# Optimization experiments

Hardware: AMD Instinct MI355X
Metric: run time of the kernel (lower is better)

Reference implementation:

```python
import jax, jax.numpy as jnp
import numpy as np

B = 16384      # batch (rollout size)
OBS = 64       # obs_dim
ACT = 8        # action_dim
H = 128        # hidden_dim
NN = 4         # num_neighbors
N = NN + 1     # num_nodes in local graph
HEADS = 2
SLOPE = 0.2    # leaky_relu negative slope


def setup_inputs() -> dict:
    key = jax.random.key(0)
    ks = jax.random.split(key, 20)

    def glorot(k, shape):
        fan_in, fan_out = shape[0], shape[-1]
        lim = np.sqrt(6.0 / (fan_in + fan_out)).astype(np.float32)
        return jax.random.uniform(k, shape, jnp.float32, -lim, lim)

    obs = jax.random.normal(ks[0], (B, OBS), jnp.float32)
    neighbor_obs = jax.random.normal(ks[1], (B, NN, OBS), jnp.float32)
    adj = jax.random.randint(ks[2], (B, N), 0, 2, jnp.int32)
    adj = adj.at[:, 0].set(1)  # self node always connected (avoids all -inf rows)

    params = dict(
        enc_w1=glorot(ks[3], (OBS, H)), enc_b1=jnp.zeros((H,), jnp.float32),
        enc_w2=glorot(ks[4], (H, H)),  enc_b2=jnp.zeros((H,), jnp.float32),
        gat_w=glorot(ks[5], (HEADS, H, H)),       # per-head W (no bias)
        gat_a=glorot(ks[6], (HEADS, 2 * H)),      # per-head attention vector a
        val_w1=glorot(ks[7], (H * HEADS, H)), val_b1=jnp.zeros((H,), jnp.float32),
        val_w2=glorot(ks[8], (H, 1)),          val_b2=jnp.zeros((1,), jnp.float32),
        pol_w1=glorot(ks[9], (H * HEADS, H)), pol_b1=jnp.zeros((H,), jnp.float32),
        pol_w2=glorot(ks[10], (H, ACT)),       pol_b2=jnp.zeros((ACT,), jnp.float32),
    )
    return {"obs": obs, "neighbor_obs": neighbor_obs, "adj": adj, **params}


def reference(obs, neighbor_obs, adj,
              enc_w1, enc_b1, enc_w2, enc_b2,
              gat_w, gat_a,
              val_w1, val_b1, val_w2, val_b2,
              pol_w1, pol_b1, pol_w2, pol_b2):
    # shared local encoder applied to self obs and each neighbor obs
    all_obs = jnp.concatenate([obs[:, None, :], neighbor_obs], axis=1)   # [B,N,OBS]
    emb = jax.nn.relu(all_obs @ enc_w1 + enc_b1) @ enc_w2 + enc_b2       # [B,N,H]

    # GAT layer (all heads vectorized). Concat attention a^T[Wh_i||Wh_j]
    # decomposes into a1.Wh_i + a2.Wh_j.
    Wh = jnp.einsum('bnd,hdo->bhno', emb, gat_w)                          # [B,heads,N,H]
    a1, a2 = gat_a[:, :H], gat_a[:, H:]
    ei = jnp.einsum('bhno,ho->bhn', Wh, a1)                               # [B,heads,N]
    ej = jnp.einsum('bhno,ho->bhn', Wh, a2)
    e = jax.nn.leaky_relu(ei[..., :, None] + ej[..., None, :], SLOPE)     # [B,heads,N,N]
    # torch masked_fill broadcasts adj [B,N] as a column mask over j
    e = jnp.where((adj == 0)[:, None, None, :], -jnp.inf, e)
    attn = jax.nn.softmax(e, axis=-1)                                     # [B,heads,N,N]
    h_prime = jnp.einsum('bhij,bhjo->bhio', attn, Wh)                     # [B,heads,N,H]

    # node 0 (the agent itself), heads concatenated (head-major order, as torch cat)
    final = h_prime[:, :, 0, :].reshape(h_prime.shape[0], HEADS * H)      # [B,heads*H]

    value = jax.nn.relu(final @ val_w1 + val_b1) @ val_w2 + val_b2        # [B,1]
    logits = jax.nn.relu(final @ pol_w1 + pol_b1) @ pol_w2 + pol_b2      # [B,ACT]
    return value, logits
```

## Files before the change

### kernel.cpp

```cpp
#include <hip/hip_runtime.h>
#include <hip/hip_bf16.h>

#define B_TOT 16384

typedef __attribute__((ext_vector_type(8))) short short8;
typedef __attribute__((ext_vector_type(4))) short short4v;
typedef __attribute__((ext_vector_type(4))) float f32x4;

__device__ __forceinline__ float bf2f(short s){
  unsigned u = ((unsigned)(unsigned short)s) << 16;
  return __uint_as_float(u);
}
__device__ __forceinline__ unsigned f2bfu(float f){
  __hip_bfloat16 h = __float2bfloat16(f);
  return (unsigned)*reinterpret_cast<unsigned short*>(&h);
}
__device__ __forceinline__ short f2bf(float f){
  __hip_bfloat16 h = __float2bfloat16(f);
  return *reinterpret_cast<short*>(&h);
}

#define MFMA16(a,b,c) __builtin_amdgcn_mfma_f32_16x16x32_bf16(a,b,c,0,0,0)

#define W_W1T   0
#define W_W2T   8192
#define W_GWT   24576
#define W_HW1T  57344
#define W_PW2T  122880
#define W_VW2   123904
#define W_NELEM 124032
#define CVEC_BYTE 248064
#define PREP_TOT  124544

__global__ void prep_weights(const float* __restrict__ enc_w1, const float* __restrict__ enc_w2,
                             const float* __restrict__ gat_w, const float* __restrict__ gat_a,
                             const float* __restrict__ val_w1, const float* __restrict__ pol_w1,
                             const float* __restrict__ pol_w2, const float* __restrict__ val_w2,
                             unsigned short* __restrict__ wt, float* __restrict__ cvec){
  int t = blockIdx.x*256 + threadIdx.x;
  if (t >= PREP_TOT) return;
  if (t < W_NELEM){
    float v; int idx;
    if (t < 8192){
      int c = t >> 6, k = t & 63;
      int G = c >> 5, r = c & 31, b = r & 1, f = r >> 1;
      idx = ((G*2 + b)*16 + f)*64 + k;
      v = enc_w1[k*128 + c];
    } else if (t < 24576){
      int u = t - 8192, c = u >> 7, k = u & 127;
      int G = c >> 5, r = c & 31, b = r & 1, f = r >> 1;
      idx = 8192 + ((G*2 + b)*16 + f)*128 + k;
      v = enc_w2[k*128 + c];
    } else if (t < 57344){
      int u = t - 24576, h = u >> 14, r2 = u & 16383, o = r2 >> 7, d = r2 & 127;
      int G = o >> 5, r = o & 31, b = r & 1, f = r >> 1;
      idx = 24576 + h*16384 + ((G*2 + b)*16 + f)*128 + d;
      v = gat_w[h*16384 + d*128 + o];
    } else if (t < 122880){
      int u = t - 57344, oc = u >> 8, k = u & 255;
      int G = oc >> 5, r = oc & 31, b = r & 1, f = r >> 1;
      idx = 57344 + ((G*2 + b)*16 + f)*256 + k;
      v = (oc < 128) ? val_w1[k*128 + oc] : pol_w1[k*128 + (oc - 128)];
    } else if (t < 123904){
      int u = t - 122880, a = u >> 7, k = u & 127;
      idx = t;
      v = pol_w2[k*8 + a];
    } else {
      idx = t;
      v = val_w2[t - 123904];
    }
    wt[idx] = (unsigned short)f2bfu(v);
  } else {
    int q = t - W_NELEM;
    int vsel = q >> 7, d = q & 127;
    int h = vsel >> 1, s2 = vsel & 1;
    const float* gw = gat_w + h*16384 + d*128;
    const float* aa = gat_a + h*256 + s2*128;
    float s = 0.f;
    #pragma unroll 4
    for (int o = 0; o < 128; ++o) s += gw[o]*aa[o];
    cvec[vsel*128 + d] = s;
  }
}

#define MIX_L   20480
#define FINAL_L 0
#define H2_L    8192
#define K_LDS   30720

__global__ __launch_bounds__(256, 4) void colight_fused(
    const float* __restrict__ obs, const float* __restrict__ nobs, const int* __restrict__ adjp,
    const float* __restrict__ enc_b1, const float* __restrict__ enc_b2,
    const float* __restrict__ val_b1, const float* __restrict__ val_b2,
    const float* __restrict__ pol_b1, const float* __restrict__ pol_b2,
    const unsigned short* __restrict__ wt_all, const float* __restrict__ cvec,
    float* __restrict__ dout)
{
  __shared__ __align__(16) char lds[K_LDS];
  const int tid  = threadIdx.x;
  const int lane = tid & 63;
  const int wv   = tid >> 6;
  const int lm   = lane & 15;
  const int grp  = lane >> 4;
  const int kb   = grp * 8;
  const int gblk = blockIdx.x * 16;

  const unsigned short* w1t  = wt_all + W_W1T;
  const unsigned short* w2t  = wt_all + W_W2T;
  const unsigned short* gwt  = wt_all + W_GWT;
  const unsigned short* hw1t = wt_all + W_HW1T;
  const unsigned short* pw2t = wt_all + W_PW2T;
  const unsigned short* vw2  = wt_all + W_VW2;

  #pragma unroll
  for (int i = 0; i < 5; ++i){
    int chunk = i*256 + tid;
    int row = chunk >> 4;
    int c4  = (chunk & 15) * 4;
    int a = row/5, n = row%5;
    const float* src = n ? (nobs + ((size_t)(gblk+a)*4 + (n-1))*64 + c4)
                         : (obs  + (size_t)(gblk+a)*64 + c4);
    float4 v = *reinterpret_cast<const float4*>(src);
    short4v p = { f2bf(v.x), f2bf(v.y), f2bf(v.z), f2bf(v.w) };
    *reinterpret_cast<short4v*>(lds + ((row*128 + c4*2) ^ ((row & 7) << 4))) = p;
  }
  __syncthreads();

  {
    f32x4 aE[5], aO[5];
    #pragma unroll
    for (int mt=0; mt<5; ++mt){ aE[mt]=(f32x4){0,0,0,0}; aO[mt]=(f32x4){0,0,0,0}; }
    #pragma unroll
    for (int ks=0; ks<2; ++ks){
      short8 bE = *reinterpret_cast<const short8*>(w1t + ((wv*2+0)*16 + lm)*64 + ks*32 + kb);
      short8 bO = *reinterpret_cast<const short8*>(w1t + ((wv*2+1)*16 + lm)*64 + ks*32 + kb);
      #pragma unroll
      for (int mt=0; mt<5; ++mt){
        int row = mt*16 + lm;
        short8 a = *reinterpret_cast<short8*>(lds + ((row*128 + (ks*32+kb)*2) ^ ((row&7)<<4)));
        aE[mt] = MFMA16(a, bE, aE[mt]);
        aO[mt] = MFMA16(a, bO, aO[mt]);
      }
    }
    const int ce = 32*wv + 2*lm;
    const float be = enc_b1[ce], bo = enc_b1[ce+1];
    #pragma unroll
    for (int mt=0; mt<5; ++mt)
      #pragma unroll
      for (int j=0; j<4; ++j){
        int row = mt*16 + grp*4 + j;
        unsigned pk = f2bfu(fmaxf(aE[mt][j] + be, 0.f))
                    | (f2bfu(fmaxf(aO[mt][j] + bo, 0.f)) << 16);
        *reinterpret_cast<unsigned*>(lds + 10240 + ((row*256 + ce*2) ^ ((row&7)<<4))) = pk;
      }
  }
  __syncthreads();

  {
    f32x4 aE[5], aO[5];
    #pragma unroll
    for (int mt=0; mt<5; ++mt){ aE[mt]=(f32x4){0,0,0,0}; aO[mt]=(f32x4){0,0,0,0}; }
    #pragma unroll
    for (int ks=0; ks<4; ++ks){
      short8 bE = *reinterpret_cast<const short8*>(w2t + ((wv*2+0)*16 + lm)*128 + ks*32 + kb);
      short8 bO = *reinterpret_cast<const short8*>(w2t + ((wv*2+1)*16 + lm)*128 + ks*32 + kb);
      #pragma unroll
      for (int mt=0; mt<5; ++mt){
        int row = mt*16 + lm;
        short8 a = *reinterpret_cast<short8*>(lds + 10240 + ((row*256 + (ks*32+kb)*2) ^ ((row&7)<<4)));
        aE[mt] = MFMA16(a, bE, aE[mt]);
        aO[mt] = MFMA16(a, bO, aO[mt]);
      }
    }
    __syncthreads();
    const int ce = 32*wv + 2*lm;
    const float be = enc_b2[ce], bo = enc_b2[ce+1];
    #pragma unroll
    for (int mt=0; mt<5; ++mt)
      #pragma unroll
      for (int j=0; j<4; ++j){
        int row = mt*16 + grp*4 + j;
        unsigned pk = f2bfu(aE[mt][j] + be) | (f2bfu(aO[mt][j] + bo) << 16);
        *reinterpret_cast<unsigned*>(lds + ((row*256 + ce*2) ^ ((row&7)<<4))) = pk;
      }
  }
  __syncthreads();

  {
    const int ag = wv*4 + grp;
    const int ga = gblk + ag;
    float ef[5][8];
    #pragma unroll
    for (int n=0; n<5; ++n){
      int row = ag*5 + n;
      short8 er = *reinterpret_cast<short8*>(lds + ((row*256 + lm*16) ^ ((row&7)<<4)));
      #pragma unroll
      for (int e=0; e<8; ++e) ef[n][e] = bf2f(er[e]);
    }
    int msk[5];
    #pragma unroll
    for (int n=0; n<5; ++n) msk[n] = adjp[(size_t)ga*5 + n];

    #pragma unroll
    for (int h=0; h<2; ++h){
      float c1v[8], c2v[8];
      #pragma unroll
      for (int e=0; e<8; ++e){
        c1v[e] = cvec[(2*h  )*128 + lm*8 + e];
        c2v[e] = cvec[(2*h+1)*128 + lm*8 + e];
      }
      float ei = 0.f;
      #pragma unroll
      for (int e=0; e<8; ++e) ei += ef[0][e]*c1v[e];
      ei += __shfl_xor(ei,1); ei += __shfl_xor(ei,2); ei += __shfl_xor(ei,4); ei += __shfl_xor(ei,8);

      float at[5]; float mx = -1e30f;
      #pragma unroll
      for (int n=0; n<5; ++n){
        float t = 0.f;
        #pragma unroll
        for (int e=0; e<8; ++e) t += ef[n][e]*c2v[e];
        t += __shfl_xor(t,1); t += __shfl_xor(t,2); t += __shfl_xor(t,4); t += __shfl_xor(t,8);
        float s = ei + t;
        s = (s > 0.f) ? s : 0.2f*s;
        at[n] = s;
        if (msk[n] && s > mx) mx = s;
      }
      float den = 0.f;
      #pragma unroll
      for (int n=0; n<5; ++n){
        float e2 = msk[n] ? __expf(at[n]-mx) : 0.f;
        at[n] = e2; den += e2;
      }
      float inv = 1.f/den;
      short8 o;
      #pragma unroll
      for (int e=0; e<8; ++e){
        float s = 0.f;
        #pragma unroll
        for (int n=0; n<5; ++n) s += at[n]*ef[n][e];
        o[e] = f2bf(s*inv);
      }
      *reinterpret_cast<short8*>(lds + MIX_L + ((ag*512 + (h*128 + lm*8)*2) ^ ((ag&7)<<4))) = o;
    }
  }
  __syncthreads();

  {
    const int hh = wv >> 1, half = wv & 1;
    f32x4 fE[2], fO[2];
    #pragma unroll
    for (int g2=0; g2<2; ++g2){ fE[g2]=(f32x4){0,0,0,0}; fO[g2]=(f32x4){0,0,0,0}; }
    #pragma unroll
    for (int ks=0; ks<4; ++ks){
      short8 a = *reinterpret_cast<short8*>(lds + MIX_L + ((lm*512 + (hh*128 + ks*32 + kb)*2) ^ ((lm&7)<<4)));
      #pragma unroll
      for (int g2=0; g2<2; ++g2){
        int G = half*2 + g2;
        short8 bE = *reinterpret_cast<const short8*>(gwt + hh*16384 + ((G*2+0)*16 + lm)*128 + ks*32 + kb);
        short8 bO = *reinterpret_cast<const short8*>(gwt + hh*16384 + ((G*2+1)*16 + lm)*128 + ks*32 + kb);
        fE[g2] = MFMA16(a, bE, fE[g2]);
        fO[g2] = MFMA16(a, bO, fO[g2]);
      }
    }
    #pragma unroll
    for (int g2=0; g2<2; ++g2){
      int cb = hh*128 + half*64 + 32*g2 + 2*lm;
      #pragma unroll
      for (int j=0; j<4; ++j){
        int row = grp*4 + j;
        unsigned pk = f2bfu(fE[g2][j]) | (f2bfu(fO[g2][j]) << 16);
        *reinterpret_cast<unsigned*>(lds + FINAL_L + ((row*512 + cb*2) ^ ((row&7)<<4))) = pk;
      }
    }
  }
  __syncthreads();

  {
    f32x4 hE[2], hO[2];
    #pragma unroll
    for (int g2=0; g2<2; ++g2){ hE[g2]=(f32x4){0,0,0,0}; hO[g2]=(f32x4){0,0,0,0}; }
    #pragma unroll
    for (int ks=0; ks<8; ++ks){
      short8 a = *reinterpret_cast<short8*>(lds + FINAL_L + ((lm*512 + (ks*32+kb)*2) ^ ((lm&7)<<4)));
      #pragma unroll
      for (int g2=0; g2<2; ++g2){
        int G = 2*wv + g2;
        short8 bE = *reinterpret_cast<const short8*>(hw1t + ((G*2+0)*16 + lm)*256 + ks*32 + kb);
        short8 bO = *reinterpret_cast<const short8*>(hw1t + ((G*2+1)*16 + lm)*256 + ks*32 + kb);
        hE[g2] = MFMA16(a, bE, hE[g2]);
        hO[g2] = MFMA16(a, bO, hO[g2]);
      }
    }
    #pragma unroll
    for (int g2=0; g2<2; ++g2){
      int oc = 64*wv + 32*g2 + 2*lm;
      float be = (oc   < 128) ? val_b1[oc]   : pol_b1[oc-128];
      float bo = (oc+1 < 128) ? val_b1[oc+1] : pol_b1[oc-127];
      #pragma unroll
      for (int j=0; j<4; ++j){
        int row = grp*4 + j;
        unsigned pk = f2bfu(fmaxf(hE[g2][j] + be, 0.f))
                    | (f2bfu(fmaxf(hO[g2][j] + bo, 0.f)) << 16);
        *reinterpret_cast<unsigned*>(lds + H2_L + ((row*512 + oc*2) ^ ((row&7)<<4))) = pk;
      }
    }
  }
  __syncthreads();

  if (tid < 128){
    int a = tid >> 3, act = tid & 7;
    float s = pol_b2[act];
    #pragma unroll
    for (int i=0; i<16; ++i){
      short8 v = *reinterpret_cast<short8*>(lds + H2_L + ((a*512 + (128 + i*8)*2) ^ ((a&7)<<4)));
      short8 w = *reinterpret_cast<const short8*>(pw2t + act*128 + i*8);
      #pragma unroll
      for (int e=0; e<8; ++e) s += bf2f(v[e]) * bf2f(w[e]);
    }
    dout[B_TOT + (size_t)(gblk + a)*8 + act] = s;
  } else if (tid < 160){
    int q = tid - 128, a = q >> 1, hf = q & 1;
    float s = 0.f;
    #pragma unroll
    for (int i=0; i<8; ++i){
      short8 v = *reinterpret_cast<short8*>(lds + H2_L + ((a*512 + (hf*64 + i*8)*2) ^ ((a&7)<<4)));
      short8 w = *reinterpret_cast<const short8*>(vw2 + hf*64 + i*8);
      #pragma unroll
      for (int e=0; e<8; ++e) s += bf2f(v[e]) * bf2f(w[e]);
    }
    s += __shfl_xor(s, 1);
    if (!hf) dout[gblk + a] = s + val_b2[0];
  }
}

extern "C" void kernel_launch(void* const* d_in, const int* in_sizes, int n_in,
                              void* d_out, int out_size, void* d_ws, size_t ws_size,
                              hipStream_t stream) {
  (void)in_sizes; (void)n_in; (void)out_size; (void)ws_size;
  const float* obs    = (const float*)d_in[0];
  const float* nobs   = (const float*)d_in[1];
  const int*   adj    = (const int*)  d_in[2];
  const float* enc_w1 = (const float*)d_in[3];
  const float* enc_b1 = (const float*)d_in[4];
  const float* enc_w2 = (const float*)d_in[5];
  const float* enc_b2 = (const float*)d_in[6];
  const float* gat_w  = (const float*)d_in[7];
  const float* gat_a  = (const float*)d_in[8];
  const float* val_w1 = (const float*)d_in[9];
  const float* val_b1 = (const float*)d_in[10];
  const float* val_w2 = (const float*)d_in[11];
  const float* val_b2 = (const float*)d_in[12];
  const float* pol_w1 = (const float*)d_in[13];
  const float* pol_b1 = (const float*)d_in[14];
  const float* pol_w2 = (const float*)d_in[15];
  const float* pol_b2 = (const float*)d_in[16];

  unsigned short* wt   = (unsigned short*)d_ws;
  float*          cvec = (float*)((char*)d_ws + CVEC_BYTE);

  prep_weights<<<(PREP_TOT + 255)/256, 256, 0, stream>>>(
      enc_w1, enc_w2, gat_w, gat_a, val_w1, pol_w1, pol_w2, val_w2, wt, cvec);

  colight_fused<<<B_TOT/16, 256, 0, stream>>>(
      obs, nobs, adj, enc_b1, enc_b2,
      val_b1, val_b2, pol_b1, pol_b2,
      wt, cvec, (float*)d_out);
}
```

Measured before the change: 136.5 us.

## Halve agents per block to 8, shrink LDS, split heads across lane groups

Each block now processes 8 agents instead of 16, doubling the grid. LDS drops from 30 KB to 15 KB and launch bounds rise to 8 waves per SIMD to raise occupancy. The attention stage assigns one head per 16-lane group instead of looping over both heads. In exchange, the encoder and head GEMMs use padded MFMA tiles: 40 rows are covered by 48 and 8 rows by 16, so some MFMA work is wasted, and weight fragments are reloaded by twice as many blocks.

```diff
diff --git a/kernel.cpp b/kernel.cpp
--- a/kernel.cpp
+++ b/kernel.cpp
@@ -63,11 +63,9 @@
       v = (oc < 128) ? val_w1[k*128 + oc] : pol_w1[k*128 + (oc - 128)];
     } else if (t < 123904){
       int u = t - 122880, a = u >> 7, k = u & 127;
-      idx = t;
-      v = pol_w2[k*8 + a];
+      idx = t; v = pol_w2[k*8 + a];
     } else {
-      idx = t;
-      v = val_w2[t - 123904];
+      idx = t; v = val_w2[t - 123904];
     }
     wt[idx] = (unsigned short)f2bfu(v);
   } else {
@@ -83,12 +81,15 @@
   }
 }
 
-#define MIX_L   20480
-#define FINAL_L 0
-#define H2_L    8192
-#define K_LDS   30720
-
-__global__ __launch_bounds__(256, 4) void colight_fused(
+#define X_L     0
+#define H1_L    5120
+#define EMB_L   0
+#define MIX_L   10240
+#define FIN_L   0
+#define H2_L    4096
+#define K_LDS   15360
+
+__global__ __launch_bounds__(256, 8) void colight_fused(
     const float* __restrict__ obs, const float* __restrict__ nobs, const int* __restrict__ adjp,
     const float* __restrict__ enc_b1, const float* __restrict__ enc_b2,
     const float* __restrict__ val_b1, const float* __restrict__ val_b2,
@@ -103,7 +104,7 @@
   const int lm   = lane & 15;
   const int grp  = lane >> 4;
   const int kb   = grp * 8;
-  const int gblk = blockIdx.x * 16;
+  const int gblk = blockIdx.x * 8;
 
   const unsigned short* w1t  = wt_all + W_W1T;
   const unsigned short* w2t  = wt_all + W_W2T;
@@ -113,31 +114,34 @@
   const unsigned short* vw2  = wt_all + W_VW2;
 
   #pragma unroll
-  for (int i = 0; i < 5; ++i){
+  for (int i = 0; i < 3; ++i){
     int chunk = i*256 + tid;
-    int row = chunk >> 4;
-    int c4  = (chunk & 15) * 4;
-    int a = row/5, n = row%5;
-    const float* src = n ? (nobs + ((size_t)(gblk+a)*4 + (n-1))*64 + c4)
-                         : (obs  + (size_t)(gblk+a)*64 + c4);
-    float4 v = *reinterpret_cast<const float4*>(src);
-    short4v p = { f2bf(v.x), f2bf(v.y), f2bf(v.z), f2bf(v.w) };
-    *reinterpret_cast<short4v*>(lds + ((row*128 + c4*2) ^ ((row & 7) << 4))) = p;
-  }
-  __syncthreads();
-
-  {
-    f32x4 aE[5], aO[5];
-    #pragma unroll
-    for (int mt=0; mt<5; ++mt){ aE[mt]=(f32x4){0,0,0,0}; aO[mt]=(f32x4){0,0,0,0}; }
+    if (chunk < 640){
+      int row = chunk >> 4;
+      int c4  = (chunk & 15) * 4;
+      int a = row/5, n = row%5;
+      const float* src = n ? (nobs + ((size_t)(gblk+a)*4 + (n-1))*64 + c4)
+                           : (obs  + (size_t)(gblk+a)*64 + c4);
+      float4 v = *reinterpret_cast<const float4*>(src);
+      short4v p = { f2bf(v.x), f2bf(v.y), f2bf(v.z), f2bf(v.w) };
+      *reinterpret_cast<short4v*>(lds + X_L + ((row*128 + c4*2) ^ ((row & 7) << 4))) = p;
+    }
+  }
+  __syncthreads();
+
+  {
+    f32x4 aE[3], aO[3];
+    #pragma unroll
+    for (int mt=0; mt<3; ++mt){ aE[mt]=(f32x4){0,0,0,0}; aO[mt]=(f32x4){0,0,0,0}; }
     #pragma unroll
     for (int ks=0; ks<2; ++ks){
       short8 bE = *reinterpret_cast<const short8*>(w1t + ((wv*2+0)*16 + lm)*64 + ks*32 + kb);
       short8 bO = *reinterpret_cast<const short8*>(w1t + ((wv*2+1)*16 + lm)*64 + ks*32 + kb);
       #pragma unroll
-      for (int mt=0; mt<5; ++mt){
+      for (int mt=0; mt<3; ++mt){
         int row = mt*16 + lm;
-        short8 a = *reinterpret_cast<short8*>(lds + ((row*128 + (ks*32+kb)*2) ^ ((row&7)<<4)));
+        if (mt == 2 && lm >= 8) row -= 16;
+        short8 a = *reinterpret_cast<short8*>(lds + X_L + ((row*128 + (ks*32+kb)*2) ^ ((row&7)<<4)));
         aE[mt] = MFMA16(a, bE, aE[mt]);
         aO[mt] = MFMA16(a, bO, aO[mt]);
       }
@@ -145,29 +149,32 @@
     const int ce = 32*wv + 2*lm;
     const float be = enc_b1[ce], bo = enc_b1[ce+1];
     #pragma unroll
-    for (int mt=0; mt<5; ++mt)
+    for (int mt=0; mt<3; ++mt)
       #pragma unroll
       for (int j=0; j<4; ++j){
         int row = mt*16 + grp*4 + j;
-        unsigned pk = f2bfu(fmaxf(aE[mt][j] + be, 0.f))
-                    | (f2bfu(fmaxf(aO[mt][j] + bo, 0.f)) << 16);
-        *reinterpret_cast<unsigned*>(lds + 10240 + ((row*256 + ce*2) ^ ((row&7)<<4))) = pk;
-      }
-  }
-  __syncthreads();
-
-  {
-    f32x4 aE[5], aO[5];
-    #pragma unroll
-    for (int mt=0; mt<5; ++mt){ aE[mt]=(f32x4){0,0,0,0}; aO[mt]=(f32x4){0,0,0,0}; }
+        if (row < 40){
+          unsigned pk = f2bfu(fmaxf(aE[mt][j] + be, 0.f))
+                      | (f2bfu(fmaxf(aO[mt][j] + bo, 0.f)) << 16);
+          *reinterpret_cast<unsigned*>(lds + H1_L + ((row*256 + ce*2) ^ ((row&7)<<4))) = pk;
+        }
+      }
+  }
+  __syncthreads();
+
+  {
+    f32x4 aE[3], aO[3];
+    #pragma unroll
+    for (int mt=0; mt<3; ++mt){ aE[mt]=(f32x4){0,0,0,0}; aO[mt]=(f32x4){0,0,0,0}; }
     #pragma unroll
     for (int ks=0; ks<4; ++ks){
       short8 bE = *reinterpret_cast<const short8*>(w2t + ((wv*2+0)*16 + lm)*128 + ks*32 + kb);
       short8 bO = *reinterpret_cast<const short8*>(w2t + ((wv*2+1)*16 + lm)*128 + ks*32 + kb);
       #pragma unroll
-      for (int mt=0; mt<5; ++mt){
+      for (int mt=0; mt<3; ++mt){
         int row = mt*16 + lm;
-        short8 a = *reinterpret_cast<short8*>(lds + 10240 + ((row*256 + (ks*32+kb)*2) ^ ((row&7)<<4)));
+        if (mt == 2 && lm >= 8) row -= 16;
+        short8 a = *reinterpret_cast<short8*>(lds + H1_L + ((row*256 + (ks*32+kb)*2) ^ ((row&7)<<4)));
         aE[mt] = MFMA16(a, bE, aE[mt]);
         aO[mt] = MFMA16(a, bO, aO[mt]);
       }
@@ -176,84 +183,89 @@
     const int ce = 32*wv + 2*lm;
     const float be = enc_b2[ce], bo = enc_b2[ce+1];
     #pragma unroll
-    for (int mt=0; mt<5; ++mt)
+    for (int mt=0; mt<3; ++mt)
       #pragma unroll
       for (int j=0; j<4; ++j){
         int row = mt*16 + grp*4 + j;
-        unsigned pk = f2bfu(aE[mt][j] + be) | (f2bfu(aO[mt][j] + bo) << 16);
-        *reinterpret_cast<unsigned*>(lds + ((row*256 + ce*2) ^ ((row&7)<<4))) = pk;
-      }
-  }
-  __syncthreads();
-
-  {
-    const int ag = wv*4 + grp;
+        if (row < 40){
+          unsigned pk = f2bfu(aE[mt][j] + be) | (f2bfu(aO[mt][j] + bo) << 16);
+          *reinterpret_cast<unsigned*>(lds + EMB_L + ((row*256 + ce*2) ^ ((row&7)<<4))) = pk;
+        }
+      }
+  }
+  __syncthreads();
+
+  {
+    const int g  = wv*4 + grp;
+    const int ag = g >> 1;
+    const int hd = g & 1;
     const int ga = gblk + ag;
     float ef[5][8];
     #pragma unroll
     for (int n=0; n<5; ++n){
       int row = ag*5 + n;
-      short8 er = *reinterpret_cast<short8*>(lds + ((row*256 + lm*16) ^ ((row&7)<<4)));
+      short8 er = *reinterpret_cast<short8*>(lds + EMB_L + ((row*256 + lm*16) ^ ((row&7)<<4)));
       #pragma unroll
       for (int e=0; e<8; ++e) ef[n][e] = bf2f(er[e]);
     }
+    float c1v[8], c2v[8];
+    {
+      const float4* cp1 = reinterpret_cast<const float4*>(cvec + (2*hd)*128 + lm*8);
+      const float4* cp2 = reinterpret_cast<const float4*>(cvec + (2*hd+1)*128 + lm*8);
+      float4 u0 = cp1[0], u1 = cp1[1], v0 = cp2[0], v1 = cp2[1];
+      c1v[0]=u0.x; c1v[1]=u0.y; c1v[2]=u0.z; c1v[3]=u0.w;
+      c1v[4]=u1.x; c1v[5]=u1.y; c1v[6]=u1.z; c1v[7]=u1.w;
+      c2v[0]=v0.x; c2v[1]=v0.y; c2v[2]=v0.z; c2v[3]=v0.w;
+      c2v[4]=v1.x; c2v[5]=v1.y; c2v[6]=v1.z; c2v[7]=v1.w;
+    }
+    float ei = 0.f;
+    #pragma unroll
+    for (int e=0; e<8; ++e) ei += ef[0][e]*c1v[e];
+    ei += __shfl_xor(ei,1); ei += __shfl_xor(ei,2); ei += __shfl_xor(ei,4); ei += __shfl_xor(ei,8);
+
+    float at[5]; float mx = -1e30f;
     int msk[5];
     #pragma unroll
     for (int n=0; n<5; ++n) msk[n] = adjp[(size_t)ga*5 + n];
-
-    #pragma unroll
-    for (int h=0; h<2; ++h){
-      float c1v[8], c2v[8];
-      #pragma unroll
-      for (int e=0; e<8; ++e){
-        c1v[e] = cvec[(2*h  )*128 + lm*8 + e];
-        c2v[e] = cvec[(2*h+1)*128 + lm*8 + e];
-      }
-      float ei = 0.f;
-      #pragma unroll
-      for (int e=0; e<8; ++e) ei += ef[0][e]*c1v[e];
-      ei += __shfl_xor(ei,1); ei += __shfl_xor(ei,2); ei += __shfl_xor(ei,4); ei += __shfl_xor(ei,8);
-
-      float at[5]; float mx = -1e30f;
-      #pragma unroll
-      for (int n=0; n<5; ++n){
-        float t = 0.f;
-        #pragma unroll
-        for (int e=0; e<8; ++e) t += ef[n][e]*c2v[e];
-        t += __shfl_xor(t,1); t += __shfl_xor(t,2); t += __shfl_xor(t,4); t += __shfl_xor(t,8);
-        float s = ei + t;
-        s = (s > 0.f) ? s : 0.2f*s;
-        at[n] = s;
-        if (msk[n] && s > mx) mx = s;
-      }
-      float den = 0.f;
-      #pragma unroll
-      for (int n=0; n<5; ++n){
-        float e2 = msk[n] ? __expf(at[n]-mx) : 0.f;
-        at[n] = e2; den += e2;
-      }
-      float inv = 1.f/den;
-      short8 o;
-      #pragma unroll
-      for (int e=0; e<8; ++e){
-        float s = 0.f;
-        #pragma unroll
-        for (int n=0; n<5; ++n) s += at[n]*ef[n][e];
-        o[e] = f2bf(s*inv);
-      }
-      *reinterpret_cast<short8*>(lds + MIX_L + ((ag*512 + (h*128 + lm*8)*2) ^ ((ag&7)<<4))) = o;
-    }
+    #pragma unroll
+    for (int n=0; n<5; ++n){
+      float t = 0.f;
+      #pragma unroll
+      for (int e=0; e<8; ++e) t += ef[n][e]*c2v[e];
+      t += __shfl_xor(t,1); t += __shfl_xor(t,2); t += __shfl_xor(t,4); t += __shfl_xor(t,8);
+      float s = ei + t;
+      s = (s > 0.f) ? s : 0.2f*s;
+      at[n] = s;
+      if (msk[n] && s > mx) mx = s;
+    }
+    float den = 0.f;
+    #pragma unroll
+    for (int n=0; n<5; ++n){
+      float e2 = msk[n] ? __expf(at[n]-mx) : 0.f;
+      at[n] = e2; den += e2;
+    }
+    float inv = 1.f/den;
+    short8 o;
+    #pragma unroll
+    for (int e=0; e<8; ++e){
+      float s = 0.f;
+      #pragma unroll
+      for (int n=0; n<5; ++n) s += at[n]*ef[n][e];
+      o[e] = f2bf(s*inv);
+    }
+    *reinterpret_cast<short8*>(lds + MIX_L + ((ag*512 + (hd*128 + lm*8)*2) ^ ((ag&7)<<4))) = o;
   }
   __syncthreads();
 
   {
     const int hh = wv >> 1, half = wv & 1;
+    const int arow = lm & 7;
     f32x4 fE[2], fO[2];
     #pragma unroll
     for (int g2=0; g2<2; ++g2){ fE[g2]=(f32x4){0,0,0,0}; fO[g2]=(f32x4){0,0,0,0}; }
     #pragma unroll
     for (int ks=0; ks<4; ++ks){
-      short8 a = *reinterpret_cast<short8*>(lds + MIX_L + ((lm*512 + (hh*128 + ks*32 + kb)*2) ^ ((lm&7)<<4)));
+      short8 a = *reinterpret_cast<short8*>(lds + MIX_L + ((arow*512 + (hh*128 + ks*32 + kb)*2) ^ ((arow&7)<<4)));
       #pragma unroll
       for (int g2=0; g2<2; ++g2){
         int G = half*2 + g2;
@@ -269,20 +281,23 @@
       #pragma unroll
       for (int j=0; j<4; ++j){
         int row = grp*4 + j;
-        unsigned pk = f2bfu(fE[g2][j]) | (f2bfu(fO[g2][j]) << 16);
-        *reinterpret_cast<unsigned*>(lds + FINAL_L + ((row*512 + cb*2) ^ ((row&7)<<4))) = pk;
-      }
-    }
-  }
-  __syncthreads();
-
-  {
+        if (row < 8){
+          unsigned pk = f2bfu(fE[g2][j]) | (f2bfu(fO[g2][j]) << 16);
+          *reinterpret_cast<unsigned*>(lds + FIN_L + ((row*512 + cb*2) ^ ((row&7)<<4))) = pk;
+        }
+      }
+    }
+  }
+  __syncthreads();
+
+  {
+    const int arow = lm & 7;
     f32x4 hE[2], hO[2];
     #pragma unroll
     for (int g2=0; g2<2; ++g2){ hE[g2]=(f32x4){0,0,0,0}; hO[g2]=(f32x4){0,0,0,0}; }
     #pragma unroll
     for (int ks=0; ks<8; ++ks){
-      short8 a = *reinterpret_cast<short8*>(lds + FINAL_L + ((lm*512 + (ks*32+kb)*2) ^ ((lm&7)<<4)));
+      short8 a = *reinterpret_cast<short8*>(lds + FIN_L + ((arow*512 + (ks*32+kb)*2) ^ ((arow&7)<<4)));
       #pragma unroll
       for (int g2=0; g2<2; ++g2){
         int G = 2*wv + g2;
@@ -300,15 +315,17 @@
       #pragma unroll
       for (int j=0; j<4; ++j){
         int row = grp*4 + j;
-        unsigned pk = f2bfu(fmaxf(hE[g2][j] + be, 0.f))
-                    | (f2bfu(fmaxf(hO[g2][j] + bo, 0.f)) << 16);
-        *reinterpret_cast<unsigned*>(lds + H2_L + ((row*512 + oc*2) ^ ((row&7)<<4))) = pk;
-      }
-    }
-  }
-  __syncthreads();
-
-  if (tid < 128){
+        if (row < 8){
+          unsigned pk = f2bfu(fmaxf(hE[g2][j] + be, 0.f))
+                      | (f2bfu(fmaxf(hO[g2][j] + bo, 0.f)) << 16);
+          *reinterpret_cast<unsigned*>(lds + H2_L + ((row*512 + oc*2) ^ ((row&7)<<4))) = pk;
+        }
+      }
+    }
+  }
+  __syncthreads();
+
+  if (tid < 64){
     int a = tid >> 3, act = tid & 7;
     float s = pol_b2[act];
     #pragma unroll
@@ -319,8 +336,8 @@
       for (int e=0; e<8; ++e) s += bf2f(v[e]) * bf2f(w[e]);
     }
     dout[B_TOT + (size_t)(gblk + a)*8 + act] = s;
-  } else if (tid < 160){
-    int q = tid - 128, a = q >> 1, hf = q & 1;
+  } else if (tid < 80){
+    int q = tid - 64, a = q >> 1, hf = q & 1;
     float s = 0.f;
     #pragma unroll
     for (int i=0; i<8; ++i){
@@ -362,7 +379,7 @@
   prep_weights<<<(PREP_TOT + 255)/256, 256, 0, stream>>>(
       enc_w1, enc_w2, gat_w, gat_a, val_w1, pol_w1, pol_w2, val_w2, wt, cvec);
 
-  colight_fused<<<B_TOT/16, 256, 0, stream>>>(
+  colight_fused<<<B_TOT/8, 256, 0, stream>>>(
       obs, nobs, adj, enc_b1, enc_b2,
       val_b1, val_b2, pol_b1, pol_b2,
       wt, cvec, (float*)d_out);
```

After: 197.6 us. 44.8% more time.
